# Kernel tuning notes

Measured on AMD Instinct MI355X. Metric: run time of the kernel, lower is better.

## Reference

```python
import jax, jax.numpy as jnp
import numpy as np
from jax import lax

H = 128

def _lstm_gates(x, h, c, w_ih, w_hh, b_ih, b_hh):
    # PyTorch gate order: i, f, g, o
    g = x @ w_ih.T + h @ w_hh.T + b_ih + b_hh
    i, f, gg, o = jnp.split(g, 4, axis=-1)
    c_new = jax.nn.sigmoid(f) * c + jax.nn.sigmoid(i) * jnp.tanh(gg)
    h_new = jax.nn.sigmoid(o) * jnp.tanh(c_new)
    return h_new, c_new

def _lstm_layer(x_btF, w_ih, w_hh, b_ih, b_hh):
    B = x_btF.shape[0]
    h0 = jnp.zeros((B, H), x_btF.dtype)
    c0 = jnp.zeros((B, H), x_btF.dtype)
    def step(carry, xt):
        h, c = carry
        h, c = _lstm_gates(xt, h, c, w_ih, w_hh, b_ih, b_hh)
        return (h, c), h
    (h_T, c_T), ys = lax.scan(step, (h0, c0), jnp.swapaxes(x_btF, 0, 1))
    return jnp.swapaxes(ys, 0, 1), h_T, c_T

def setup_inputs() -> dict:
    key = jax.random.key(0)
    ks = jax.random.split(key, 20)
    B, T, D, P = 4096, 200, 2, 3
    s = 1.0 / np.sqrt(H)
    u = lambda k, shp: jax.random.uniform(k, shp, jnp.float32, -s, s)
    return {
        'x_hist': jax.random.normal(ks[0], (B, T, D), jnp.float32),
        'params': jax.random.normal(ks[1], (B, P), jnp.float32),
        'pred_len': 200,
        'w_ih0': u(ks[2], (4 * H, D)), 'w_hh0': u(ks[3], (4 * H, H)),
        'b_ih0': u(ks[4], (4 * H,)), 'b_hh0': u(ks[5], (4 * H,)),
        'w_ih1': u(ks[6], (4 * H, H)), 'w_hh1': u(ks[7], (4 * H, H)),
        'b_ih1': u(ks[8], (4 * H,)), 'b_hh1': u(ks[9], (4 * H,)),
        'dec_w_ih': u(ks[10], (4 * H, D + P)), 'dec_w_hh': u(ks[11], (4 * H, H)),
        'dec_b_ih': u(ks[12], (4 * H,)), 'dec_b_hh': u(ks[13], (4 * H,)),
        'proj_w': u(ks[14], (H, P)), 'proj_b': u(ks[15], (H,)),
        'out_w': u(ks[16], (2, H)), 'out_b': u(ks[17], (2,)),
    }

def reference(x_hist, params, pred_len, w_ih0, w_hh0, b_ih0, b_hh0,
              w_ih1, w_hh1, b_ih1, b_hh1, dec_w_ih, dec_w_hh, dec_b_ih,
              dec_b_hh, proj_w, proj_b, out_w, out_b):
    # 2-layer encoder LSTM; only last layer's final (h, c) are used
    y1, _, _ = _lstm_layer(x_hist, w_ih0, w_hh0, b_ih0, b_hh0)
    _, h_n, c_n = _lstm_layer(y1, w_ih1, w_hh1, b_ih1, b_hh1)
    h = h_n + params @ proj_w.T + proj_b
    c = c_n
    cur = x_hist[:, -1, :]
    def step(carry, _):
        h, c, cur = carry
        inp = jnp.concatenate([cur, params], axis=-1)
        h, c = _lstm_gates(inp, h, c, dec_w_ih, dec_w_hh, dec_b_ih, dec_b_hh)
        cur = h @ out_w.T + out_b
        return (h, c, cur), cur
    _, preds = lax.scan(step, (h, c, cur), None, length=pred_len)
    return jnp.swapaxes(preds, 0, 1)  # [B, pred_len, 2]
```

## Files before the change

### kernel.cpp

```cpp
#include <hip/hip_runtime.h>
#include <stdint.h>

typedef __bf16 bf16x8 __attribute__((ext_vector_type(8)));
typedef float  f32x4  __attribute__((ext_vector_type(4)));

#define PRED   200
#define TSTEPS 200
#define NBLK   256
#define ASTR   280
#define ALO    136
#define ABUFB  (16*ASTR*2)
#define W_BYTES 131072
#define A_OFF   W_BYTES
#define LDS_A   (A_OFF + 2*ABUFB)
#define STG_OFF (A_OFF + 2*ABUFB)
#define LDS_C   (STG_OFF + ABUFB)
#define CP_OFF  (A_OFF + 2*ABUFB)
#define CUR_OFF (CP_OFF + 1024)
#define LDS_D   (CUR_OFF + 128)

#define STATE_FLOATS ((size_t)NBLK*4*2048)

__device__ __forceinline__ float sigm(float x){ return 1.0f/(1.0f+__expf(-x)); }
__device__ __forceinline__ float tanhx(float x){
  float t=__expf(-2.0f*fabsf(x)); float y=(1.0f-t)/(1.0f+t); return copysignf(y,x);
}
__device__ __forceinline__ bf16x8 hi8(float4 a, float4 b){
  bf16x8 r; r[0]=(__bf16)a.x; r[1]=(__bf16)a.y; r[2]=(__bf16)a.z; r[3]=(__bf16)a.w;
  r[4]=(__bf16)b.x; r[5]=(__bf16)b.y; r[6]=(__bf16)b.z; r[7]=(__bf16)b.w; return r;
}
__device__ __forceinline__ bf16x8 lo8(float4 a, float4 b, bf16x8 h){
  bf16x8 r;
  r[0]=(__bf16)(a.x-(float)h[0]); r[1]=(__bf16)(a.y-(float)h[1]);
  r[2]=(__bf16)(a.z-(float)h[2]); r[3]=(__bf16)(a.w-(float)h[3]);
  r[4]=(__bf16)(b.x-(float)h[4]); r[5]=(__bf16)(b.y-(float)h[5]);
  r[6]=(__bf16)(b.z-(float)h[6]); r[7]=(__bf16)(b.w-(float)h[7]); return r;
}
#define MFMA(A,B,C) __builtin_amdgcn_mfma_f32_16x16x32_bf16((A),(B),(C),0,0,0)

__global__ void __launch_bounds__(512,2)
k_l0(const float* __restrict__ xh, const float* __restrict__ wih0,
     const float* __restrict__ whh0, const float* __restrict__ bih0,
     const float* __restrict__ bhh0, float* __restrict__ wsf,
     int chunkStart, int chunkLen, unsigned long long stageFloats)
{
  extern __shared__ char smem[];
  const int tid=threadIdx.x, wv=tid>>6, l=tid&63, c=l&15, qd=l>>4;
  const int hc=wv*16+c, blk=blockIdx.x, r0=blk*16;
  float* stf = wsf + stageFloats;
  #pragma unroll
  for (int i=0;i<16;++i){
    int f=i*8+wv, ntg=f>>2, kt=f&3;
    int g=(ntg&3)*128+(ntg>>2)*16+c, k=kt*32+qd*8;
    const float* s=whh0+g*128+k;
    *(bf16x8*)(smem+f*1024+l*16)=hi8(*(const float4*)s,*(const float4*)(s+4));
  }
  bf16x8 wlo[16];
  #pragma unroll
  for (int tt=0;tt<4;++tt)
    #pragma unroll
    for (int kt=0;kt<4;++kt){
      const float* s=whh0+(size_t)(tt*128+hc)*128+kt*32+qd*8;
      float4 a=*(const float4*)s, b=*(const float4*)(s+4);
      wlo[tt*4+kt]=lo8(a,b,hi8(a,b));
    }
  float b0[4], w0x[4], w0y[4];
  #pragma unroll
  for (int tt=0;tt<4;++tt){
    int g=tt*128+hc;
    b0[tt]=bih0[g]+bhh0[g]; w0x[tt]=wih0[2*g]; w0y[tt]=wih0[2*g+1];
  }
  float c0[4];
  {
    __bf16* B1=(__bf16*)(smem+A_OFF+ABUFB);
    const float* hst=stf+(size_t)(blk*4+0)*2048;
    const float* cst=stf+(size_t)(blk*4+1)*2048;
    #pragma unroll
    for (int i=0;i<4;++i){
      int e=tid*4+i, row=e>>7, col=e&127;
      float v=0.f; if(chunkStart) v=hst[e];
      __bf16 h=(__bf16)v;
      B1[row*ASTR+col]=h; B1[row*ASTR+ALO+col]=(__bf16)(v-(float)h);
    }
    #pragma unroll
    for (int j=0;j<4;++j){ float v=0.f; if(chunkStart) v=cst[(qd*4+j)*128+hc]; c0[j]=v; }
  }
  __syncthreads();
  for (int t=0;t<chunkLen;++t){
    const int p=t&1, tg=chunkStart+t;
    float2 xv[4];
    #pragma unroll
    for (int j=0;j<4;++j) xv[j]=*(const float2*)(xh+(size_t)(r0+qd*4+j)*400+tg*2);
    f32x4 acc[4];
    #pragma unroll
    for (int tt=0;tt<4;++tt) acc[tt]=(f32x4){b0[tt],b0[tt],b0[tt],b0[tt]};
    const char* Ar=smem+A_OFF+(size_t)(1-p)*ABUFB;
    #pragma unroll
    for (int kt=0;kt<4;++kt){
      bf16x8 ah=*(const bf16x8*)(Ar+(c*ASTR+kt*32+qd*8)*2);
      bf16x8 al=*(const bf16x8*)(Ar+(c*ASTR+ALO+kt*32+qd*8)*2);
      #pragma unroll
      for (int tt=0;tt<4;++tt){
        bf16x8 bh=*(const bf16x8*)(smem+(size_t)((wv*4+tt)*4+kt)*1024+l*16);
        acc[tt]=MFMA(ah,bh,acc[tt]);
        acc[tt]=MFMA(al,bh,acc[tt]);
        acc[tt]=MFMA(ah,wlo[tt*4+kt],acc[tt]);
      }
    }
    __bf16* Aw=(__bf16*)(smem+A_OFF+(size_t)p*ABUFB);
    float* h0o=wsf+((size_t)t*NBLK+blk)*2048;
    #pragma unroll
    for (int j=0;j<4;++j){
      float gi=acc[0][j]+xv[j].x*w0x[0]+xv[j].y*w0y[0];
      float gf=acc[1][j]+xv[j].x*w0x[1]+xv[j].y*w0y[1];
      float gg=acc[2][j]+xv[j].x*w0x[2]+xv[j].y*w0y[2];
      float go=acc[3][j]+xv[j].x*w0x[3]+xv[j].y*w0y[3];
      float cn=sigm(gf)*c0[j]+sigm(gi)*tanhx(gg); c0[j]=cn;
      float hn=sigm(go)*tanhx(cn);
      int row=qd*4+j;
      __bf16 hh=(__bf16)hn;
      Aw[row*ASTR+hc]=hh; Aw[row*ASTR+ALO+hc]=(__bf16)(hn-(float)hh);
      h0o[row*128+hc]=hn;
      if (t==chunkLen-1){
        stf[(size_t)(blk*4+0)*2048+row*128+hc]=hn;
        stf[(size_t)(blk*4+1)*2048+row*128+hc]=cn;
      }
    }
    __syncthreads();
  }
}

__global__ void __launch_bounds__(512,2)
k_l1(const float* __restrict__ wih1, const float* __restrict__ whh1,
     const float* __restrict__ bih1, const float* __restrict__ bhh1,
     float* __restrict__ wsf, int chunkStart, int chunkLen,
     unsigned long long stageFloats)
{
  extern __shared__ char smem[];
  const int tid=threadIdx.x, wv=tid>>6, l=tid&63, c=l&15, qd=l>>4;
  const int hc=wv*16+c, blk=blockIdx.x;
  float* stf = wsf + stageFloats;
  #pragma unroll
  for (int i=0;i<16;++i){
    int f=i*8+wv, ntg=f>>2, kt=f&3;
    int g=(ntg&3)*128+(ntg>>2)*16+c, k=kt*32+qd*8;
    const float* s=wih1+g*128+k;
    *(bf16x8*)(smem+f*1024+l*16)=hi8(*(const float4*)s,*(const float4*)(s+4));
  }
  bf16x8 whh[16], whl[16];
  #pragma unroll
  for (int tt=0;tt<4;++tt)
    #pragma unroll
    for (int kt=0;kt<4;++kt){
      const float* s2=whh1+(size_t)(tt*128+hc)*128+kt*32+qd*8;
      float4 a2=*(const float4*)s2, b2=*(const float4*)(s2+4);
      bf16x8 h2=hi8(a2,b2);
      whh[tt*4+kt]=h2; whl[tt*4+kt]=lo8(a2,b2,h2);
    }
  float b1v[4];
  #pragma unroll
  for (int tt=0;tt<4;++tt){ int g=tt*128+hc; b1v[tt]=bih1[g]+bhh1[g]; }
  float c1[4];
  {
    __bf16* B1=(__bf16*)(smem+A_OFF+ABUFB);
    const float* hst=stf+(size_t)(blk*4+2)*2048;
    const float* cst=stf+(size_t)(blk*4+3)*2048;
    #pragma unroll
    for (int i=0;i<4;++i){
      int e=tid*4+i, row=e>>7, col=e&127;
      float v=0.f; if(chunkStart) v=hst[e];
      __bf16 h=(__bf16)v;
      B1[row*ASTR+col]=h; B1[row*ASTR+ALO+col]=(__bf16)(v-(float)h);
    }
    #pragma unroll
    for (int j=0;j<4;++j){ float v=0.f; if(chunkStart) v=cst[(qd*4+j)*128+hc]; c1[j]=v; }
  }
  float4 r4=*(const float4*)(wsf+((size_t)0*NBLK+blk)*2048+tid*4);
  __syncthreads();
  for (int t=0;t<chunkLen;++t){
    const int p=t&1;
    {
      __bf16* ST=(__bf16*)(smem+STG_OFF);
      int e=tid*4, row=e>>7, col=e&127;
      #pragma unroll
      for (int i=0;i<4;++i){
        float v=r4[i]; __bf16 h=(__bf16)v;
        ST[row*ASTR+col+i]=h; ST[row*ASTR+ALO+col+i]=(__bf16)(v-(float)h);
      }
    }
    if (t+1<chunkLen) r4=*(const float4*)(wsf+((size_t)(t+1)*NBLK+blk)*2048+tid*4);
    __syncthreads();
    f32x4 acc[4];
    #pragma unroll
    for (int tt=0;tt<4;++tt) acc[tt]=(f32x4){b1v[tt],b1v[tt],b1v[tt],b1v[tt]};
    const char* Ar=smem+A_OFF+(size_t)(1-p)*ABUFB;
    const char* Sr=smem+STG_OFF;
    #pragma unroll
    for (int kt=0;kt<4;++kt){
      bf16x8 a0h=*(const bf16x8*)(Sr+(c*ASTR+kt*32+qd*8)*2);
      bf16x8 a0l=*(const bf16x8*)(Sr+(c*ASTR+ALO+kt*32+qd*8)*2);
      bf16x8 a1h=*(const bf16x8*)(Ar+(c*ASTR+kt*32+qd*8)*2);
      bf16x8 a1l=*(const bf16x8*)(Ar+(c*ASTR+ALO+kt*32+qd*8)*2);
      #pragma unroll
      for (int tt=0;tt<4;++tt){
        bf16x8 bh=*(const bf16x8*)(smem+(size_t)((wv*4+tt)*4+kt)*1024+l*16);
        const float* sw=wih1+(size_t)(tt*128+hc)*128+kt*32+qd*8;
        float4 wa=*(const float4*)sw, wb=*(const float4*)(sw+4);
        bf16x8 wl=lo8(wa,wb,hi8(wa,wb));
        acc[tt]=MFMA(a0h,bh,acc[tt]);
        acc[tt]=MFMA(a0l,bh,acc[tt]);
        acc[tt]=MFMA(a0h,wl,acc[tt]);
        acc[tt]=MFMA(a1h,whh[tt*4+kt],acc[tt]);
        acc[tt]=MFMA(a1l,whh[tt*4+kt],acc[tt]);
        acc[tt]=MFMA(a1h,whl[tt*4+kt],acc[tt]);
      }
    }
    __bf16* Aw=(__bf16*)(smem+A_OFF+(size_t)p*ABUFB);
    #pragma unroll
    for (int j=0;j<4;++j){
      float cn=sigm(acc[1][j])*c1[j]+sigm(acc[0][j])*tanhx(acc[2][j]); c1[j]=cn;
      float hn=sigm(acc[3][j])*tanhx(cn);
      int row=qd*4+j;
      __bf16 hh=(__bf16)hn;
      Aw[row*ASTR+hc]=hh; Aw[row*ASTR+ALO+hc]=(__bf16)(hn-(float)hh);
      if (t==chunkLen-1){
        stf[(size_t)(blk*4+2)*2048+row*128+hc]=hn;
        stf[(size_t)(blk*4+3)*2048+row*128+hc]=cn;
      }
    }
    __syncthreads();
  }
}

__global__ void __launch_bounds__(512,2)
k_dec(const float* __restrict__ xh, const float* __restrict__ pprm,
      const float* __restrict__ dwihp, const float* __restrict__ dwhh,
      const float* __restrict__ dbih, const float* __restrict__ dbhh,
      const float* __restrict__ pw, const float* __restrict__ pb,
      const float* __restrict__ ow, const float* __restrict__ ob,
      const float* __restrict__ wsf, float* __restrict__ out,
      unsigned long long stageFloats)
{
  extern __shared__ char smem[];
  const int tid=threadIdx.x, wv=tid>>6, l=tid&63, c=l&15, qd=l>>4;
  const int hc=wv*16+c, blk=blockIdx.x, r0=blk*16;
  const float* stf = wsf + stageFloats;
  #pragma unroll
  for (int i=0;i<16;++i){
    int f=i*8+wv, ntg=f>>2, kt=f&3;
    int g=(ntg&3)*128+(ntg>>2)*16+c, k=kt*32+qd*8;
    const float* s=dwhh+g*128+k;
    *(bf16x8*)(smem+f*1024+l*16)=hi8(*(const float4*)s,*(const float4*)(s+4));
  }
  bf16x8 wlo[16];
  #pragma unroll
  for (int tt=0;tt<4;++tt)
    #pragma unroll
    for (int kt=0;kt<4;++kt){
      const float* s=dwhh+(size_t)(tt*128+hc)*128+kt*32+qd*8;
      float4 a=*(const float4*)s, b=*(const float4*)(s+4);
      wlo[tt*4+kt]=lo8(a,b,hi8(a,b));
    }
  float dwi[4][5], db[4];
  #pragma unroll
  for (int tt=0;tt<4;++tt){
    int g=tt*128+hc;
    db[tt]=dbih[g]+dbhh[g];
    #pragma unroll
    for (int k=0;k<5;++k) dwi[tt][k]=dwihp[g*5+k];
  }
  float prj0=pw[hc*3+0], prj1=pw[hc*3+1], prj2=pw[hc*3+2], prjb=pb[hc];
  float ow0=ow[hc], ow1=ow[128+hc];
  float prm[4][3];
  #pragma unroll
  for (int j=0;j<4;++j){
    size_t r=(size_t)(r0+qd*4+j);
    prm[j][0]=pprm[r*3+0]; prm[j][1]=pprm[r*3+1]; prm[j][2]=pprm[r*3+2];
  }
  const float* h1s=stf+(size_t)(blk*4+2)*2048;
  const float* c1s=stf+(size_t)(blk*4+3)*2048;
  float c1[4];
  {
    __bf16* B0=(__bf16*)(smem+A_OFF);
    #pragma unroll
    for (int j=0;j<4;++j){
      int row=qd*4+j;
      float hd=h1s[row*128+hc]+prm[j][0]*prj0+prm[j][1]*prj1+prm[j][2]*prj2+prjb;
      __bf16 h=(__bf16)hd;
      B0[row*ASTR+hc]=h; B0[row*ASTR+ALO+hc]=(__bf16)(hd-(float)h);
      c1[j]=c1s[row*128+hc];
    }
  }
  float obv=0.f;
  if (tid<32){
    int r=tid>>1, d=tid&1;
    ((float*)(smem+CUR_OFF))[tid]=xh[(size_t)(r0+r)*400+199*2+d];
    obv=ob[d];
  }
  __syncthreads();
  for (int s=0;s<PRED;++s){
    const int q=s&1;
    float cur0[4], cur1[4];
    #pragma unroll
    for (int j=0;j<4;++j){
      cur0[j]=((const float*)(smem+CUR_OFF))[(qd*4+j)*2+0];
      cur1[j]=((const float*)(smem+CUR_OFF))[(qd*4+j)*2+1];
    }
    f32x4 acc[4];
    #pragma unroll
    for (int tt=0;tt<4;++tt) acc[tt]=(f32x4){db[tt],db[tt],db[tt],db[tt]};
    const char* Ar=smem+A_OFF+(size_t)q*ABUFB;
    #pragma unroll
    for (int kt=0;kt<4;++kt){
      bf16x8 ah=*(const bf16x8*)(Ar+(c*ASTR+kt*32+qd*8)*2);
      bf16x8 al=*(const bf16x8*)(Ar+(c*ASTR+ALO+kt*32+qd*8)*2);
      #pragma unroll
      for (int tt=0;tt<4;++tt){
        bf16x8 bh=*(const bf16x8*)(smem+(size_t)((wv*4+tt)*4+kt)*1024+l*16);
        acc[tt]=MFMA(ah,bh,acc[tt]);
        acc[tt]=MFMA(al,bh,acc[tt]);
        acc[tt]=MFMA(ah,wlo[tt*4+kt],acc[tt]);
      }
    }
    __bf16* Aw=(__bf16*)(smem+A_OFF+(size_t)(1-q)*ABUFB);
    float pc0[4], pc1[4];
    #pragma unroll
    for (int j=0;j<4;++j){
      float gi=acc[0][j]+cur0[j]*dwi[0][0]+cur1[j]*dwi[0][1]+prm[j][0]*dwi[0][2]+prm[j][1]*dwi[0][3]+prm[j][2]*dwi[0][4];
      float gf=acc[1][j]+cur0[j]*dwi[1][0]+cur1[j]*dwi[1][1]+prm[j][0]*dwi[1][2]+prm[j][1]*dwi[1][3]+prm[j][2]*dwi[1][4];
      float gg=acc[2][j]+cur0[j]*dwi[2][0]+cur1[j]*dwi[2][1]+prm[j][0]*dwi[2][2]+prm[j][1]*dwi[2][3]+prm[j][2]*dwi[2][4];
      float go=acc[3][j]+cur0[j]*dwi[3][0]+cur1[j]*dwi[3][1]+prm[j][0]*dwi[3][2]+prm[j][1]*dwi[3][3]+prm[j][2]*dwi[3][4];
      float cn=sigm(gf)*c1[j]+sigm(gi)*tanhx(gg); c1[j]=cn;
      float hn=sigm(go)*tanhx(cn);
      int row=qd*4+j;
      __bf16 hh=(__bf16)hn;
      Aw[row*ASTR+hc]=hh; Aw[row*ASTR+ALO+hc]=(__bf16)(hn-(float)hh);
      pc0[j]=hn*ow0; pc1[j]=hn*ow1;
    }
    #pragma unroll
    for (int m=1;m<16;m<<=1){
      #pragma unroll
      for (int j=0;j<4;++j){
        pc0[j]+=__shfl_xor(pc0[j],m,64);
        pc1[j]+=__shfl_xor(pc1[j],m,64);
      }
    }
    float* cp=(float*)(smem+CP_OFF);
    if (c==0){
      #pragma unroll
      for (int j=0;j<4;++j){
        cp[(wv*16+qd*4+j)*2+0]=pc0[j];
        cp[(wv*16+qd*4+j)*2+1]=pc1[j];
      }
    }
    __syncthreads();
    if (tid<32){
      int r=tid>>1, d=tid&1;
      float sv=obv;
      #pragma unroll
      for (int w2=0;w2<8;++w2) sv+=cp[(w2*16+r)*2+d];
      ((float*)(smem+CUR_OFF))[tid]=sv;
      out[(size_t)(r0+r)*400+s*2+d]=sv;
    }
    __syncthreads();
  }
}

extern "C" void kernel_launch(void* const* d_in, const int* in_sizes, int n_in,
                              void* d_out, int out_size, void* d_ws, size_t ws_size,
                              hipStream_t stream)
{
  (void)out_size;
  const int base = (n_in >= 19 && in_sizes[2] == 1) ? 3 : 2;
  const float* xh   = (const float*)d_in[0];
  const float* prm  = (const float*)d_in[1];
  const float* wih0 = (const float*)d_in[base+0];
  const float* whh0 = (const float*)d_in[base+1];
  const float* bih0 = (const float*)d_in[base+2];
  const float* bhh0 = (const float*)d_in[base+3];
  const float* wih1 = (const float*)d_in[base+4];
  const float* whh1 = (const float*)d_in[base+5];
  const float* bih1 = (const float*)d_in[base+6];
  const float* bhh1 = (const float*)d_in[base+7];
  const float* dwih = (const float*)d_in[base+8];
  const float* dwhh = (const float*)d_in[base+9];
  const float* dbih = (const float*)d_in[base+10];
  const float* dbhh = (const float*)d_in[base+11];
  const float* pw   = (const float*)d_in[base+12];
  const float* pb   = (const float*)d_in[base+13];
  const float* ow   = (const float*)d_in[base+14];
  const float* ob   = (const float*)d_in[base+15];
  float* wsf = (float*)d_ws;

  size_t wsFloats = ws_size / 4;
  size_t avail = (wsFloats > STATE_FLOATS) ? (wsFloats - STATE_FLOATS) : 0;
  int chunkLen = (int)(avail / ((size_t)NBLK * 2048));
  if (chunkLen > 50) chunkLen = 50;
  if (chunkLen < 1)  chunkLen = 1;
  unsigned long long stageFloats = (unsigned long long)chunkLen * NBLK * 2048;

  hipFuncSetAttribute((const void*)k_l0,  hipFuncAttributeMaxDynamicSharedMemorySize, LDS_A);
  hipFuncSetAttribute((const void*)k_l1,  hipFuncAttributeMaxDynamicSharedMemorySize, LDS_C);
  hipFuncSetAttribute((const void*)k_dec, hipFuncAttributeMaxDynamicSharedMemorySize, LDS_D);

  for (int k0 = 0; k0 < TSTEPS; k0 += chunkLen){
    int len = chunkLen; if (k0 + len > TSTEPS) len = TSTEPS - k0;
    k_l0<<<NBLK,512,LDS_A,stream>>>(xh, wih0, whh0, bih0, bhh0, wsf, k0, len, stageFloats);
    k_l1<<<NBLK,512,LDS_C,stream>>>(wih1, whh1, bih1, bhh1, wsf, k0, len, stageFloats);
  }
  k_dec<<<NBLK,512,LDS_D,stream>>>(xh, prm, dwih, dwhh, dbih, dbhh,
                                   pw, pb, ow, ob, wsf, (float*)d_out, stageFloats);
}
```

Measured before the change: 1.956 ms.

## Swizzle LDS state layout, keep weights in registers, fuse output projection via MFMA

Replaces the padded activation buffers with an XOR-swizzled 512-byte-row LDS layout to avoid bank conflicts. Moves the hi part of the recurrent weights from LDS into registers for layer 0 and the decoder, which shrinks their LDS footprint. Layer 1 now keeps the ih low part in registers instead of reloading and converting it from global memory every step. The decoder folds the params and bias terms into a precomputed accumulator init and computes the output projection with extra MFMAs, dropping the shuffle reduction, the cross-wave LDS reduction and one barrier per step. The cost is much higher register pressure, which risks spills under the 512x2 launch bounds.

```diff
diff --git a/kernel.cpp b/kernel.cpp
--- a/kernel.cpp
+++ b/kernel.cpp
@@ -7,17 +7,11 @@
 #define PRED   200
 #define TSTEPS 200
 #define NBLK   256
-#define ASTR   280
-#define ALO    136
-#define ABUFB  (16*ASTR*2)
-#define W_BYTES 131072
-#define A_OFF   W_BYTES
-#define LDS_A   (A_OFF + 2*ABUFB)
-#define STG_OFF (A_OFF + 2*ABUFB)
-#define LDS_C   (STG_OFF + ABUFB)
-#define CP_OFF  (A_OFF + 2*ABUFB)
-#define CUR_OFF (CP_OFF + 1024)
-#define LDS_D   (CUR_OFF + 128)
+#define ABUFB  8192
+#define L1_A_OFF   131072
+#define L1_ST_OFF  (131072 + 2*ABUFB)
+#define LDS_L1     (131072 + 3*ABUFB)
+#define LDS_SMALL  (2*ABUFB)
 
 #define STATE_FLOATS ((size_t)NBLK*4*2048)
 
@@ -37,6 +31,13 @@
   r[6]=(__bf16)(b.z-(float)h[6]); r[7]=(__bf16)(b.w-(float)h[7]); return r;
 }
 #define MFMA(A,B,C) __builtin_amdgcn_mfma_f32_16x16x32_bf16((A),(B),(C),0,0,0)
+
+__device__ __forceinline__ int aoff(int row, int col){
+  return row*512 + ((((col>>3) ^ (row&7)) << 4) | ((col&7)<<1));
+}
+__device__ __forceinline__ int frdoff(int c, int qd, int kt, int plane){
+  return c*512 + (((((kt<<2)+qd) ^ (c&7)) | (plane<<4)) << 4);
+}
 
 __global__ void __launch_bounds__(512,2)
 k_l0(const float* __restrict__ xh, const float* __restrict__ wih0,
@@ -48,21 +49,14 @@
   const int tid=threadIdx.x, wv=tid>>6, l=tid&63, c=l&15, qd=l>>4;
   const int hc=wv*16+c, blk=blockIdx.x, r0=blk*16;
   float* stf = wsf + stageFloats;
-  #pragma unroll
-  for (int i=0;i<16;++i){
-    int f=i*8+wv, ntg=f>>2, kt=f&3;
-    int g=(ntg&3)*128+(ntg>>2)*16+c, k=kt*32+qd*8;
-    const float* s=whh0+g*128+k;
-    *(bf16x8*)(smem+f*1024+l*16)=hi8(*(const float4*)s,*(const float4*)(s+4));
-  }
-  bf16x8 wlo[16];
+  bf16x8 whi[16], wlo[16];
   #pragma unroll
   for (int tt=0;tt<4;++tt)
     #pragma unroll
     for (int kt=0;kt<4;++kt){
       const float* s=whh0+(size_t)(tt*128+hc)*128+kt*32+qd*8;
       float4 a=*(const float4*)s, b=*(const float4*)(s+4);
-      wlo[tt*4+kt]=lo8(a,b,hi8(a,b));
+      whi[tt*4+kt]=hi8(a,b); wlo[tt*4+kt]=lo8(a,b,whi[tt*4+kt]);
     }
   float b0[4], w0x[4], w0y[4];
   #pragma unroll
@@ -72,7 +66,7 @@
   }
   float c0[4];
   {
-    __bf16* B1=(__bf16*)(smem+A_OFF+ABUFB);
+    char* B1=smem+ABUFB;
     const float* hst=stf+(size_t)(blk*4+0)*2048;
     const float* cst=stf+(size_t)(blk*4+1)*2048;
     #pragma unroll
@@ -80,7 +74,8 @@
       int e=tid*4+i, row=e>>7, col=e&127;
       float v=0.f; if(chunkStart) v=hst[e];
       __bf16 h=(__bf16)v;
-      B1[row*ASTR+col]=h; B1[row*ASTR+ALO+col]=(__bf16)(v-(float)h);
+      *(__bf16*)(B1+aoff(row,col))=h;
+      *(__bf16*)(B1+aoff(row,col+128))=(__bf16)(v-(float)h);
     }
     #pragma unroll
     for (int j=0;j<4;++j){ float v=0.f; if(chunkStart) v=cst[(qd*4+j)*128+hc]; c0[j]=v; }
@@ -94,20 +89,19 @@
     f32x4 acc[4];
     #pragma unroll
     for (int tt=0;tt<4;++tt) acc[tt]=(f32x4){b0[tt],b0[tt],b0[tt],b0[tt]};
-    const char* Ar=smem+A_OFF+(size_t)(1-p)*ABUFB;
-    #pragma unroll
-    for (int kt=0;kt<4;++kt){
-      bf16x8 ah=*(const bf16x8*)(Ar+(c*ASTR+kt*32+qd*8)*2);
-      bf16x8 al=*(const bf16x8*)(Ar+(c*ASTR+ALO+kt*32+qd*8)*2);
+    const char* Ar=smem+(size_t)(1-p)*ABUFB;
+    #pragma unroll
+    for (int kt=0;kt<4;++kt){
+      bf16x8 ah=*(const bf16x8*)(Ar+frdoff(c,qd,kt,0));
+      bf16x8 al=*(const bf16x8*)(Ar+frdoff(c,qd,kt,1));
       #pragma unroll
       for (int tt=0;tt<4;++tt){
-        bf16x8 bh=*(const bf16x8*)(smem+(size_t)((wv*4+tt)*4+kt)*1024+l*16);
-        acc[tt]=MFMA(ah,bh,acc[tt]);
-        acc[tt]=MFMA(al,bh,acc[tt]);
+        acc[tt]=MFMA(ah,whi[tt*4+kt],acc[tt]);
+        acc[tt]=MFMA(al,whi[tt*4+kt],acc[tt]);
         acc[tt]=MFMA(ah,wlo[tt*4+kt],acc[tt]);
       }
     }
-    __bf16* Aw=(__bf16*)(smem+A_OFF+(size_t)p*ABUFB);
+    char* Aw=smem+(size_t)p*ABUFB;
     float* h0o=wsf+((size_t)t*NBLK+blk)*2048;
     #pragma unroll
     for (int j=0;j<4;++j){
@@ -119,7 +113,8 @@
       float hn=sigm(go)*tanhx(cn);
       int row=qd*4+j;
       __bf16 hh=(__bf16)hn;
-      Aw[row*ASTR+hc]=hh; Aw[row*ASTR+ALO+hc]=(__bf16)(hn-(float)hh);
+      *(__bf16*)(Aw+aoff(row,hc))=hh;
+      *(__bf16*)(Aw+aoff(row,hc+128))=(__bf16)(hn-(float)hh);
       h0o[row*128+hc]=hn;
       if (t==chunkLen-1){
         stf[(size_t)(blk*4+0)*2048+row*128+hc]=hn;
@@ -147,11 +142,14 @@
     const float* s=wih1+g*128+k;
     *(bf16x8*)(smem+f*1024+l*16)=hi8(*(const float4*)s,*(const float4*)(s+4));
   }
-  bf16x8 whh[16], whl[16];
+  bf16x8 wil[16], whh[16], whl[16];
   #pragma unroll
   for (int tt=0;tt<4;++tt)
     #pragma unroll
     for (int kt=0;kt<4;++kt){
+      const float* s=wih1+(size_t)(tt*128+hc)*128+kt*32+qd*8;
+      float4 a=*(const float4*)s, b=*(const float4*)(s+4);
+      wil[tt*4+kt]=lo8(a,b,hi8(a,b));
       const float* s2=whh1+(size_t)(tt*128+hc)*128+kt*32+qd*8;
       float4 a2=*(const float4*)s2, b2=*(const float4*)(s2+4);
       bf16x8 h2=hi8(a2,b2);
@@ -162,7 +160,7 @@
   for (int tt=0;tt<4;++tt){ int g=tt*128+hc; b1v[tt]=bih1[g]+bhh1[g]; }
   float c1[4];
   {
-    __bf16* B1=(__bf16*)(smem+A_OFF+ABUFB);
+    char* B1=smem+L1_A_OFF+ABUFB;
     const float* hst=stf+(size_t)(blk*4+2)*2048;
     const float* cst=stf+(size_t)(blk*4+3)*2048;
     #pragma unroll
@@ -170,7 +168,8 @@
       int e=tid*4+i, row=e>>7, col=e&127;
       float v=0.f; if(chunkStart) v=hst[e];
       __bf16 h=(__bf16)v;
-      B1[row*ASTR+col]=h; B1[row*ASTR+ALO+col]=(__bf16)(v-(float)h);
+      *(__bf16*)(B1+aoff(row,col))=h;
+      *(__bf16*)(B1+aoff(row,col+128))=(__bf16)(v-(float)h);
     }
     #pragma unroll
     for (int j=0;j<4;++j){ float v=0.f; if(chunkStart) v=cst[(qd*4+j)*128+hc]; c1[j]=v; }
@@ -180,12 +179,13 @@
   for (int t=0;t<chunkLen;++t){
     const int p=t&1;
     {
-      __bf16* ST=(__bf16*)(smem+STG_OFF);
+      char* ST=smem+L1_ST_OFF;
       int e=tid*4, row=e>>7, col=e&127;
       #pragma unroll
       for (int i=0;i<4;++i){
         float v=r4[i]; __bf16 h=(__bf16)v;
-        ST[row*ASTR+col+i]=h; ST[row*ASTR+ALO+col+i]=(__bf16)(v-(float)h);
+        *(__bf16*)(ST+aoff(row,col+i))=h;
+        *(__bf16*)(ST+aoff(row,col+i+128))=(__bf16)(v-(float)h);
       }
     }
     if (t+1<chunkLen) r4=*(const float4*)(wsf+((size_t)(t+1)*NBLK+blk)*2048+tid*4);
@@ -193,36 +193,34 @@
     f32x4 acc[4];
     #pragma unroll
     for (int tt=0;tt<4;++tt) acc[tt]=(f32x4){b1v[tt],b1v[tt],b1v[tt],b1v[tt]};
-    const char* Ar=smem+A_OFF+(size_t)(1-p)*ABUFB;
-    const char* Sr=smem+STG_OFF;
-    #pragma unroll
-    for (int kt=0;kt<4;++kt){
-      bf16x8 a0h=*(const bf16x8*)(Sr+(c*ASTR+kt*32+qd*8)*2);
-      bf16x8 a0l=*(const bf16x8*)(Sr+(c*ASTR+ALO+kt*32+qd*8)*2);
-      bf16x8 a1h=*(const bf16x8*)(Ar+(c*ASTR+kt*32+qd*8)*2);
-      bf16x8 a1l=*(const bf16x8*)(Ar+(c*ASTR+ALO+kt*32+qd*8)*2);
+    const char* Ar=smem+L1_A_OFF+(size_t)(1-p)*ABUFB;
+    const char* Sr=smem+L1_ST_OFF;
+    #pragma unroll
+    for (int kt=0;kt<4;++kt){
+      bf16x8 a0h=*(const bf16x8*)(Sr+frdoff(c,qd,kt,0));
+      bf16x8 a0l=*(const bf16x8*)(Sr+frdoff(c,qd,kt,1));
+      bf16x8 a1h=*(const bf16x8*)(Ar+frdoff(c,qd,kt,0));
+      bf16x8 a1l=*(const bf16x8*)(Ar+frdoff(c,qd,kt,1));
       #pragma unroll
       for (int tt=0;tt<4;++tt){
         bf16x8 bh=*(const bf16x8*)(smem+(size_t)((wv*4+tt)*4+kt)*1024+l*16);
-        const float* sw=wih1+(size_t)(tt*128+hc)*128+kt*32+qd*8;
-        float4 wa=*(const float4*)sw, wb=*(const float4*)(sw+4);
-        bf16x8 wl=lo8(wa,wb,hi8(wa,wb));
         acc[tt]=MFMA(a0h,bh,acc[tt]);
         acc[tt]=MFMA(a0l,bh,acc[tt]);
-        acc[tt]=MFMA(a0h,wl,acc[tt]);
+        acc[tt]=MFMA(a0h,wil[tt*4+kt],acc[tt]);
         acc[tt]=MFMA(a1h,whh[tt*4+kt],acc[tt]);
         acc[tt]=MFMA(a1l,whh[tt*4+kt],acc[tt]);
         acc[tt]=MFMA(a1h,whl[tt*4+kt],acc[tt]);
       }
     }
-    __bf16* Aw=(__bf16*)(smem+A_OFF+(size_t)p*ABUFB);
+    char* Aw=smem+L1_A_OFF+(size_t)p*ABUFB;
     #pragma unroll
     for (int j=0;j<4;++j){
       float cn=sigm(acc[1][j])*c1[j]+sigm(acc[0][j])*tanhx(acc[2][j]); c1[j]=cn;
       float hn=sigm(acc[3][j])*tanhx(cn);
       int row=qd*4+j;
       __bf16 hh=(__bf16)hn;
-      Aw[row*ASTR+hc]=hh; Aw[row*ASTR+ALO+hc]=(__bf16)(hn-(float)hh);
+      *(__bf16*)(Aw+aoff(row,hc))=hh;
+      *(__bf16*)(Aw+aoff(row,hc+128))=(__bf16)(hn-(float)hh);
       if (t==chunkLen-1){
         stf[(size_t)(blk*4+2)*2048+row*128+hc]=hn;
         stf[(size_t)(blk*4+3)*2048+row*128+hc]=cn;
@@ -245,124 +243,127 @@
   const int tid=threadIdx.x, wv=tid>>6, l=tid&63, c=l&15, qd=l>>4;
   const int hc=wv*16+c, blk=blockIdx.x, r0=blk*16;
   const float* stf = wsf + stageFloats;
-  #pragma unroll
-  for (int i=0;i<16;++i){
-    int f=i*8+wv, ntg=f>>2, kt=f&3;
-    int g=(ntg&3)*128+(ntg>>2)*16+c, k=kt*32+qd*8;
-    const float* s=dwhh+g*128+k;
-    *(bf16x8*)(smem+f*1024+l*16)=hi8(*(const float4*)s,*(const float4*)(s+4));
-  }
-  bf16x8 wlo[16];
+  bf16x8 whi[16], wlo[16];
   #pragma unroll
   for (int tt=0;tt<4;++tt)
     #pragma unroll
     for (int kt=0;kt<4;++kt){
       const float* s=dwhh+(size_t)(tt*128+hc)*128+kt*32+qd*8;
       float4 a=*(const float4*)s, b=*(const float4*)(s+4);
-      wlo[tt*4+kt]=lo8(a,b,hi8(a,b));
-    }
-  float dwi[4][5], db[4];
-  #pragma unroll
-  for (int tt=0;tt<4;++tt){
-    int g=tt*128+hc;
-    db[tt]=dbih[g]+dbhh[g];
-    #pragma unroll
-    for (int k=0;k<5;++k) dwi[tt][k]=dwihp[g*5+k];
-  }
-  float prj0=pw[hc*3+0], prj1=pw[hc*3+1], prj2=pw[hc*3+2], prjb=pb[hc];
-  float ow0=ow[hc], ow1=ow[128+hc];
+      whi[tt*4+kt]=hi8(a,b); wlo[tt*4+kt]=lo8(a,b,whi[tt*4+kt]);
+    }
+  bf16x8 owh[4], owl[4];
+  #pragma unroll
+  for (int kt=0;kt<4;++kt){
+    int cc=(c<2)?c:0;
+    const float* s=ow+cc*128+kt*32+qd*8;
+    float4 a=*(const float4*)s, b=*(const float4*)(s+4);
+    if (c>=2){ a=(float4){0,0,0,0}; b=(float4){0,0,0,0}; }
+    owh[kt]=hi8(a,b); owl[kt]=lo8(a,b,owh[kt]);
+  }
+  float ob0=ob[0], ob1=ob[1];
   float prm[4][3];
   #pragma unroll
   for (int j=0;j<4;++j){
     size_t r=(size_t)(r0+qd*4+j);
     prm[j][0]=pprm[r*3+0]; prm[j][1]=pprm[r*3+1]; prm[j][2]=pprm[r*3+2];
   }
+  float pt[4][4], dw0[4], dw1[4];
+  #pragma unroll
+  for (int tt=0;tt<4;++tt){
+    int g=tt*128+hc;
+    float db=dbih[g]+dbhh[g];
+    dw0[tt]=dwihp[g*5+0]; dw1[tt]=dwihp[g*5+1];
+    #pragma unroll
+    for (int j=0;j<4;++j)
+      pt[tt][j]=db+prm[j][0]*dwihp[g*5+2]+prm[j][1]*dwihp[g*5+3]+prm[j][2]*dwihp[g*5+4];
+  }
   const float* h1s=stf+(size_t)(blk*4+2)*2048;
   const float* c1s=stf+(size_t)(blk*4+3)*2048;
-  float c1[4];
+  float c1[4], cx0[4], cx1[4];
   {
-    __bf16* B0=(__bf16*)(smem+A_OFF);
+    float prj0=pw[hc*3+0], prj1=pw[hc*3+1], prj2=pw[hc*3+2], prjb=pb[hc];
+    char* B0=smem;
     #pragma unroll
     for (int j=0;j<4;++j){
       int row=qd*4+j;
       float hd=h1s[row*128+hc]+prm[j][0]*prj0+prm[j][1]*prj1+prm[j][2]*prj2+prjb;
       __bf16 h=(__bf16)hd;
-      B0[row*ASTR+hc]=h; B0[row*ASTR+ALO+hc]=(__bf16)(hd-(float)h);
+      *(__bf16*)(B0+aoff(row,hc))=h;
+      *(__bf16*)(B0+aoff(row,hc+128))=(__bf16)(hd-(float)h);
       c1[j]=c1s[row*128+hc];
-    }
-  }
-  float obv=0.f;
-  if (tid<32){
-    int r=tid>>1, d=tid&1;
-    ((float*)(smem+CUR_OFF))[tid]=xh[(size_t)(r0+r)*400+199*2+d];
-    obv=ob[d];
+      float2 xx=*(const float2*)(xh+(size_t)(r0+row)*400+398);
+      cx0[j]=xx.x; cx1[j]=xx.y;
+    }
   }
   __syncthreads();
   for (int s=0;s<PRED;++s){
     const int q=s&1;
+    const char* Ar=smem+(size_t)q*ABUFB;
+    f32x4 acc[4], accPV={0.f,0.f,0.f,0.f};
+    #pragma unroll
+    for (int tt=0;tt<4;++tt) acc[tt]=(f32x4){pt[tt][0],pt[tt][1],pt[tt][2],pt[tt][3]};
+    #pragma unroll
+    for (int kt=0;kt<4;++kt){
+      bf16x8 ah=*(const bf16x8*)(Ar+frdoff(c,qd,kt,0));
+      bf16x8 al=*(const bf16x8*)(Ar+frdoff(c,qd,kt,1));
+      #pragma unroll
+      for (int tt=0;tt<4;++tt){
+        acc[tt]=MFMA(ah,whi[tt*4+kt],acc[tt]);
+        acc[tt]=MFMA(al,whi[tt*4+kt],acc[tt]);
+        acc[tt]=MFMA(ah,wlo[tt*4+kt],acc[tt]);
+      }
+      accPV=MFMA(ah,owh[kt],accPV);
+      accPV=MFMA(al,owh[kt],accPV);
+      accPV=MFMA(ah,owl[kt],accPV);
+    }
     float cur0[4], cur1[4];
     #pragma unroll
     for (int j=0;j<4;++j){
-      cur0[j]=((const float*)(smem+CUR_OFF))[(qd*4+j)*2+0];
-      cur1[j]=((const float*)(smem+CUR_OFF))[(qd*4+j)*2+1];
-    }
-    f32x4 acc[4];
-    #pragma unroll
-    for (int tt=0;tt<4;++tt) acc[tt]=(f32x4){db[tt],db[tt],db[tt],db[tt]};
-    const char* Ar=smem+A_OFF+(size_t)q*ABUFB;
-    #pragma unroll
-    for (int kt=0;kt<4;++kt){
-      bf16x8 ah=*(const bf16x8*)(Ar+(c*ASTR+kt*32+qd*8)*2);
-      bf16x8 al=*(const bf16x8*)(Ar+(c*ASTR+ALO+kt*32+qd*8)*2);
-      #pragma unroll
-      for (int tt=0;tt<4;++tt){
-        bf16x8 bh=*(const bf16x8*)(smem+(size_t)((wv*4+tt)*4+kt)*1024+l*16);
-        acc[tt]=MFMA(ah,bh,acc[tt]);
-        acc[tt]=MFMA(al,bh,acc[tt]);
-        acc[tt]=MFMA(ah,wlo[tt*4+kt],acc[tt]);
-      }
-    }
-    __bf16* Aw=(__bf16*)(smem+A_OFF+(size_t)(1-q)*ABUFB);
-    float pc0[4], pc1[4];
+      float pv0=__shfl(accPV[j], (l&48),   64);
+      float pv1=__shfl(accPV[j], (l&48)|1, 64);
+      cur0[j]= s ? (pv0+ob0) : cx0[j];
+      cur1[j]= s ? (pv1+ob1) : cx1[j];
+    }
+    if (s && wv==0 && c<2){
+      float obv=c?ob1:ob0;
+      #pragma unroll
+      for (int j=0;j<4;++j)
+        out[(size_t)(r0+qd*4+j)*400+(s-1)*2+c]=accPV[j]+obv;
+    }
+    char* Aw=smem+(size_t)(1-q)*ABUFB;
     #pragma unroll
     for (int j=0;j<4;++j){
-      float gi=acc[0][j]+cur0[j]*dwi[0][0]+cur1[j]*dwi[0][1]+prm[j][0]*dwi[0][2]+prm[j][1]*dwi[0][3]+prm[j][2]*dwi[0][4];
-      float gf=acc[1][j]+cur0[j]*dwi[1][0]+cur1[j]*dwi[1][1]+prm[j][0]*dwi[1][2]+prm[j][1]*dwi[1][3]+prm[j][2]*dwi[1][4];
-      float gg=acc[2][j]+cur0[j]*dwi[2][0]+cur1[j]*dwi[2][1]+prm[j][0]*dwi[2][2]+prm[j][1]*dwi[2][3]+prm[j][2]*dwi[2][4];
-      float go=acc[3][j]+cur0[j]*dwi[3][0]+cur1[j]*dwi[3][1]+prm[j][0]*dwi[3][2]+prm[j][1]*dwi[3][3]+prm[j][2]*dwi[3][4];
+      float gi=acc[0][j]+cur0[j]*dw0[0]+cur1[j]*dw1[0];
+      float gf=acc[1][j]+cur0[j]*dw0[1]+cur1[j]*dw1[1];
+      float gg=acc[2][j]+cur0[j]*dw0[2]+cur1[j]*dw1[2];
+      float go=acc[3][j]+cur0[j]*dw0[3]+cur1[j]*dw1[3];
       float cn=sigm(gf)*c1[j]+sigm(gi)*tanhx(gg); c1[j]=cn;
       float hn=sigm(go)*tanhx(cn);
       int row=qd*4+j;
       __bf16 hh=(__bf16)hn;
-      Aw[row*ASTR+hc]=hh; Aw[row*ASTR+ALO+hc]=(__bf16)(hn-(float)hh);
-      pc0[j]=hn*ow0; pc1[j]=hn*ow1;
-    }
-    #pragma unroll
-    for (int m=1;m<16;m<<=1){
-      #pragma unroll
-      for (int j=0;j<4;++j){
-        pc0[j]+=__shfl_xor(pc0[j],m,64);
-        pc1[j]+=__shfl_xor(pc1[j],m,64);
-      }
-    }
-    float* cp=(float*)(smem+CP_OFF);
-    if (c==0){
-      #pragma unroll
-      for (int j=0;j<4;++j){
-        cp[(wv*16+qd*4+j)*2+0]=pc0[j];
-        cp[(wv*16+qd*4+j)*2+1]=pc1[j];
-      }
+      *(__bf16*)(Aw+aoff(row,hc))=hh;
+      *(__bf16*)(Aw+aoff(row,hc+128))=(__bf16)(hn-(float)hh);
     }
     __syncthreads();
-    if (tid<32){
-      int r=tid>>1, d=tid&1;
-      float sv=obv;
-      #pragma unroll
-      for (int w2=0;w2<8;++w2) sv+=cp[(w2*16+r)*2+d];
-      ((float*)(smem+CUR_OFF))[tid]=sv;
-      out[(size_t)(r0+r)*400+s*2+d]=sv;
-    }
-    __syncthreads();
+  }
+  {
+    const char* Ar=smem+(size_t)(PRED&1)*ABUFB;
+    f32x4 accPV={0.f,0.f,0.f,0.f};
+    #pragma unroll
+    for (int kt=0;kt<4;++kt){
+      bf16x8 ah=*(const bf16x8*)(Ar+frdoff(c,qd,kt,0));
+      bf16x8 al=*(const bf16x8*)(Ar+frdoff(c,qd,kt,1));
+      accPV=MFMA(ah,owh[kt],accPV);
+      accPV=MFMA(al,owh[kt],accPV);
+      accPV=MFMA(ah,owl[kt],accPV);
+    }
+    if (wv==0 && c<2){
+      float obv=c?ob1:ob0;
+      #pragma unroll
+      for (int j=0;j<4;++j)
+        out[(size_t)(r0+qd*4+j)*400+(PRED-1)*2+c]=accPV[j]+obv;
+    }
   }
 }
 
@@ -399,15 +400,13 @@
   if (chunkLen < 1)  chunkLen = 1;
   unsigned long long stageFloats = (unsigned long long)chunkLen * NBLK * 2048;
 
-  hipFuncSetAttribute((const void*)k_l0,  hipFuncAttributeMaxDynamicSharedMemorySize, LDS_A);
-  hipFuncSetAttribute((const void*)k_l1,  hipFuncAttributeMaxDynamicSharedMemorySize, LDS_C);
-  hipFuncSetAttribute((const void*)k_dec, hipFuncAttributeMaxDynamicSharedMemorySize, LDS_D);
+  hipFuncSetAttribute((const void*)k_l1, hipFuncAttributeMaxDynamicSharedMemorySize, LDS_L1);
 
   for (int k0 = 0; k0 < TSTEPS; k0 += chunkLen){
     int len = chunkLen; if (k0 + len > TSTEPS) len = TSTEPS - k0;
-    k_l0<<<NBLK,512,LDS_A,stream>>>(xh, wih0, whh0, bih0, bhh0, wsf, k0, len, stageFloats);
-    k_l1<<<NBLK,512,LDS_C,stream>>>(wih1, whh1, bih1, bhh1, wsf, k0, len, stageFloats);
-  }
-  k_dec<<<NBLK,512,LDS_D,stream>>>(xh, prm, dwih, dwhh, dbih, dbhh,
-                                   pw, pb, ow, ob, wsf, (float*)d_out, stageFloats);
-}
+    k_l0<<<NBLK,512,LDS_SMALL,stream>>>(xh, wih0, whh0, bih0, bhh0, wsf, k0, len, stageFloats);
+    k_l1<<<NBLK,512,LDS_L1,stream>>>(wih1, whh1, bih1, bhh1, wsf, k0, len, stageFloats);
+  }
+  k_dec<<<NBLK,512,LDS_SMALL,stream>>>(xh, prm, dwih, dwhh, dbih, dbhh,
+                                       pw, pb, ow, ob, wsf, (float*)d_out, stageFloats);
+}
```

After: 2.047 ms. 4.7% more time.
